# Performance work log

Measured on AMD Instinct MI355X. Metric: run time of the kernel, lower is better.

Reference implementation:

```python
import jax, jax.numpy as jnp
import numpy as np


def setup_inputs() -> dict:
    key = jax.random.key(0)
    ks = jax.random.split(key, 6)
    B, C, H, W = 8, 512, 64, 64
    s = 1.0 / np.sqrt(C)
    return {
        "x": jax.random.normal(ks[0], (B, C, H, W), dtype=jnp.float32),
        "w_phi": jax.random.normal(ks[1], (C, C), dtype=jnp.float32) * s,
        "w_theta": jax.random.normal(ks[2], (C, C), dtype=jnp.float32) * s,
        "w_g": jax.random.normal(ks[3], (C, C), dtype=jnp.float32) * s,
        "w_mask": jax.random.normal(ks[4], (C, C), dtype=jnp.float32) * s,
        "gamma": jax.random.normal(ks[5], (1,), dtype=jnp.float32) * 0.1,
    }


def reference(x, w_phi, w_theta, w_g, w_mask, gamma):
    b, c, h, w = x.shape
    n = h * w
    xf = x.reshape(b, c, n)  # flatten spatial: [b, c, n]
    # 1x1 convs (bias=False) are channel-mixing GEMMs
    phi = jnp.einsum("oc,bcn->bon", w_phi, xf)    # [b, c, n]
    theta = jnp.einsum("oc,bcn->bon", w_theta, xf)  # [b, c, n]
    g = jnp.einsum("oc,bcn->bon", w_g, xf)        # [b, c, n]
    # channel-channel attention (unscaled), softmax over last dim
    attn = jax.nn.softmax(jnp.einsum("bcn,bdn->bcd", phi, theta), axis=-1)  # [b, c, c]
    y = jnp.einsum("bcd,bdn->bcn", attn, g)  # [b, c, n]
    # faithful to torch: permute(0,2,1).contiguous().view(b, c, h, w)
    y = jnp.transpose(y, (0, 2, 1)).reshape(b, c, h, w)
    mask = jnp.einsum("oc,bchw->bohw", w_mask, y)
    return mask * gamma[0] + x
```

## Files before the change

### kernel.cpp

```cpp
#include <hip/hip_runtime.h>
#include <hip/hip_bf16.h>

constexpr int BATCH = 8;
constexpr int C = 512;
constexpr int HW = 4096;
constexpr long CN = (long)C * HW;
constexpr long CC = (long)C * C;

typedef __attribute__((ext_vector_type(8))) short short8;
typedef __attribute__((ext_vector_type(4))) short bf16x4;
typedef __attribute__((ext_vector_type(4))) float f32x4;

__device__ __forceinline__ void gload16(const void* g, void* l) {
  __builtin_amdgcn_global_load_lds(
      (const __attribute__((address_space(1))) void*)g,
      (__attribute__((address_space(3))) void*)l, 16, 0, 0);
}

__device__ __forceinline__ void hilo(float v, __hip_bfloat16& h, __hip_bfloat16& l) {
  h = __float2bfloat16(v);
  l = __float2bfloat16(v - __bfloat162float(h));
}
__device__ __forceinline__ short bfs(float v) {
  __hip_bfloat16 h = __float2bfloat16(v);
  return *(short*)&h;
}

__global__ __launch_bounds__(256) void convx_k(
    const float* __restrict__ x, __hip_bfloat16* __restrict__ xhi,
    __hip_bfloat16* __restrict__ xt) {
  const int b = blockIdx.z;
  const int n0 = blockIdx.x * 64, c0 = blockIdx.y * 64;
  const float* xb = x + (long)b * CN;
  __shared__ short t[64 * 65];
  const int tid = threadIdx.x;
#pragma unroll
  for (int it = 0; it < 2; ++it) {
    int slot = it * 256 + tid;
    int r = slot >> 3, cc = (slot & 7) * 8;
    const float* src = xb + (long)(c0 + r) * HW + n0 + cc;
    f32x4 v0 = *(const f32x4*)src, v1 = *(const f32x4*)(src + 4);
    short8 hh;
#pragma unroll
    for (int e = 0; e < 4; ++e) {
      hh[e] = bfs(v0[e]);
      hh[4 + e] = bfs(v1[e]);
    }
    long idx = (long)b * CN + (long)(c0 + r) * HW + n0 + cc;
    *(short8*)((short*)xhi + idx) = hh;
#pragma unroll
    for (int e = 0; e < 8; ++e) t[r * 65 + cc + e] = hh[e];
  }
  __syncthreads();
#pragma unroll
  for (int it = 0; it < 2; ++it) {
    int slot = it * 256 + tid;
    int r = slot >> 3, cc = (slot & 7) * 8;
    short8 o;
#pragma unroll
    for (int e = 0; e < 8; ++e) o[e] = t[(cc + e) * 65 + r];
    *(short8*)((short*)xt + (long)b * CN + (long)(n0 + r) * C + c0 + cc) = o;
  }
}

__global__ __launch_bounds__(256) void wprep_k(
    const float* __restrict__ wphi, const float* __restrict__ wtheta,
    const float* __restrict__ wg, const float* __restrict__ wmask,
    __hip_bfloat16* __restrict__ wph, __hip_bfloat16* __restrict__ wpl,
    __hip_bfloat16* __restrict__ wth, __hip_bfloat16* __restrict__ wtl,
    __hip_bfloat16* __restrict__ wgT, __hip_bfloat16* __restrict__ wm16) {
  const int z = blockIdx.z;
  const int r0 = blockIdx.y * 64, c0 = blockIdx.x * 64;
  const int tid = threadIdx.x;
  if (z == 2) {
    __shared__ __hip_bfloat16 t[64][65];
#pragma unroll
    for (int i = 0; i < 16; ++i) {
      int e = i * 256 + tid;
      int r = e >> 6, c = e & 63;
      t[r][c] = __float2bfloat16(wg[(long)(r0 + r) * C + c0 + c]);
    }
    __syncthreads();
#pragma unroll
    for (int i = 0; i < 16; ++i) {
      int e = i * 256 + tid;
      int r = e >> 6, c = e & 63;
      wgT[(long)(c0 + r) * C + r0 + c] = t[c][r];
    }
  } else {
#pragma unroll
    for (int i = 0; i < 16; ++i) {
      int e = i * 256 + tid;
      int r = e >> 6, c = e & 63;
      long idx = (long)(r0 + r) * C + c0 + c;
      if (z == 0) {
        __hip_bfloat16 h, l;
        hilo(wphi[idx], h, l);
        wph[idx] = h; wpl[idx] = l;
      } else if (z == 1) {
        __hip_bfloat16 h, l;
        hilo(wtheta[idx], h, l);
        wth[idx] = h; wtl[idx] = l;
      } else {
        wm16[idx] = __float2bfloat16(wmask[idx]);
      }
    }
  }
}

__global__ __launch_bounds__(256) void gram_k(
    const __hip_bfloat16* __restrict__ xhi, float* __restrict__ gpart) {
  const int b = blockIdx.z;
  const int ks = blockIdx.y;
  int i = 0, rem = blockIdx.x;
  while (rem >= 4 - i) { rem -= 4 - i; ++i; }
  const int j = i + rem;
  const int m0 = i * 128, n0 = j * 128;

  const short* X = (const short*)(xhi + (long)b * CN);
  __shared__ short lds[2 * 2 * 128 * 64];
  const int tid = threadIdx.x, w = tid >> 6, lane = tid & 63;

  f32x4 acc[4][4] = {};
  const int wr = (w >> 1) * 64, wc = (w & 1) * 64;
  const int kbeg = ks * 512;

  auto STAGE = [&](int buf, int k0) {
    short* lb = lds + buf * 16384;
#pragma unroll
    for (int it = 0; it < 8; ++it) {
      int slot = (w & 1) * 512 + it * 64 + lane;
      int r = slot >> 3, p = slot & 7, c = p ^ (r & 7);
      int gr = (w < 2) ? (m0 + r) : (n0 + r);
      gload16(X + (long)gr * HW + k0 + c * 8, lb + ((w >> 1) * 1024 + slot) * 8);
    }
  };

  STAGE(0, kbeg);
  asm volatile("s_waitcnt vmcnt(0)" ::: "memory");
  __builtin_amdgcn_s_barrier();

  for (int t = 0; t < 8; ++t) {
    if (t < 7) STAGE((t + 1) & 1, kbeg + (t + 1) * 64);
    const short* lb = lds + (t & 1) * 16384;
#pragma unroll
    for (int kh = 0; kh < 2; ++kh) {
      short8 af[4], bfr[4];
      const int ch = kh * 4 + (lane >> 4);
#pragma unroll
      for (int mi = 0; mi < 4; ++mi) {
        int r = wr + mi * 16 + (lane & 15);
        af[mi] = *(const short8*)(lb + (r * 8 + (ch ^ (r & 7))) * 8);
      }
#pragma unroll
      for (int ni = 0; ni < 4; ++ni) {
        int r = wc + ni * 16 + (lane & 15);
        bfr[ni] = *(const short8*)(lb + 8192 + (r * 8 + (ch ^ (r & 7))) * 8);
      }
#pragma unroll
      for (int mi = 0; mi < 4; ++mi)
#pragma unroll
        for (int ni = 0; ni < 4; ++ni)
          acc[mi][ni] = __builtin_amdgcn_mfma_f32_16x16x32_bf16(af[mi], bfr[ni], acc[mi][ni], 0, 0, 0);
    }
    asm volatile("s_waitcnt vmcnt(0)" ::: "memory");
    __builtin_amdgcn_s_barrier();
  }

  float* P = gpart + ((((long)b * 10 + blockIdx.x) * 8 + ks) << 14);
#pragma unroll
  for (int mi = 0; mi < 4; ++mi)
#pragma unroll
    for (int ni = 0; ni < 4; ++ni)
#pragma unroll
      for (int rr = 0; rr < 4; ++rr) {
        int row = wr + mi * 16 + (lane >> 4) * 4 + rr;
        int col = wc + ni * 16 + (lane & 15);
        P[row * 128 + col] = acc[mi][ni][rr];
      }
}

__global__ __launch_bounds__(256) void gred_k(
    const float* __restrict__ gpart, __hip_bfloat16* __restrict__ gh,
    __hip_bfloat16* __restrict__ gl) {
  const int b = blockIdx.z;
  const int half = blockIdx.y;
  int i = 0, rem = blockIdx.x;
  while (rem >= 4 - i) { rem -= 4 - i; ++i; }
  const int j = i + rem;
  const int m0 = i * 128, n0 = j * 128;
  const float* P = gpart + (((long)b * 10 + blockIdx.x) << 17) + half * 8192;
  __shared__ float T[128][65];
  const int tid = threadIdx.x;
  const long dbase = (long)b * CC;

#pragma unroll
  for (int q = 0; q < 8; ++q) {
    int e = q * 1024 + tid * 4;
    int r = e >> 7, c = e & 127;
    f32x4 s = {};
#pragma unroll
    for (int ks = 0; ks < 8; ++ks) s += *(const f32x4*)(P + (ks << 14) + e);
    bf16x4 hh, ll;
#pragma unroll
    for (int u = 0; u < 4; ++u) {
      __hip_bfloat16 h, l;
      hilo(s[u], h, l);
      hh[u] = *(short*)&h;
      ll[u] = *(short*)&l;
      T[c + u][r] = s[u];
    }
    long idx = dbase + (long)(m0 + half * 64 + r) * 512 + n0 + c;
    *(bf16x4*)((short*)gh + idx) = hh;
    *(bf16x4*)((short*)gl + idx) = ll;
  }
  if (i != j) {
    __syncthreads();
#pragma unroll
    for (int q = 0; q < 8; ++q) {
      int e = q * 1024 + tid * 4;
      int rp = e >> 6, cp = e & 63;
      bf16x4 hh, ll;
#pragma unroll
      for (int u = 0; u < 4; ++u) {
        __hip_bfloat16 h, l;
        hilo(T[rp][cp + u], h, l);
        hh[u] = *(short*)&h;
        ll[u] = *(short*)&l;
      }
      long idx = dbase + (long)(n0 + rp) * 512 + m0 + half * 64 + cp;
      *(bf16x4*)((short*)gh + idx) = hh;
      *(bf16x4*)((short*)gl + idx) = ll;
    }
  }
}

template <int AH, int BH, int EPI>
__global__ __launch_bounds__(256) void nt_small(
    const __hip_bfloat16* __restrict__ Ah_, const __hip_bfloat16* __restrict__ Al_,
    const __hip_bfloat16* __restrict__ Bh_, const __hip_bfloat16* __restrict__ Bl_,
    long aStr, long bStr, void* __restrict__ out1, void* __restrict__ out2) {
  const int b = blockIdx.z;
  const int m0 = blockIdx.y * 64, n0 = blockIdx.x * 64;
  const short* Ahp = (const short*)(Ah_ + (long)b * aStr);
  const short* Alp = AH ? (const short*)(Al_ + (long)b * aStr) : nullptr;
  const short* Bhp = (const short*)(Bh_ + (long)b * bStr);
  const short* Blp = BH ? (const short*)(Bl_ + (long)b * bStr) : nullptr;
  constexpr int PAN = (AH && BH) ? 4 : 2;
  __shared__ short lds[2 * PAN * 4096];
  const int tid = threadIdx.x, w = tid >> 6, lane = tid & 63;

  f32x4 acc[2][2] = {};
  const int wr = (w >> 1) * 32, wc = (w & 1) * 32;

  auto STAGE = [&](int buf, int k0) {
    short* lb = lds + buf * PAN * 4096;
    if constexpr (AH && BH) {
      const short* src = (w == 0) ? Ahp : (w == 1) ? Alp : (w == 2) ? Bhp : Blp;
      const int rowbase = (w & 2) ? n0 : m0;
      short* lt = lb + w * 4096;
#pragma unroll
      for (int it = 0; it < 8; ++it) {
        int slot = it * 64 + lane;
        int r = slot >> 3, p = slot & 7, c = p ^ (r & 7);
        gload16(src + (long)(rowbase + r) * 512 + k0 + c * 8, lt + slot * 8);
      }
    } else {
      const short* src = (w < 2) ? Ahp : Bhp;
      const int rowbase = (w < 2) ? m0 : n0;
      short* lt = lb + (w >> 1) * 4096;
#pragma unroll
      for (int it = 0; it < 4; ++it) {
        int slot = (w & 1) * 256 + it * 64 + lane;
        int r = slot >> 3, p = slot & 7, c = p ^ (r & 7);
        gload16(src + (long)(rowbase + r) * 512 + k0 + c * 8, lt + slot * 8);
      }
    }
  };

  STAGE(0, 0);
  asm volatile("s_waitcnt vmcnt(0)" ::: "memory");
  __builtin_amdgcn_s_barrier();

  for (int t = 0; t < 8; ++t) {
    if (t < 7) STAGE((t + 1) & 1, (t + 1) * 64);
    const short* lb = lds + (t & 1) * PAN * 4096;
#pragma unroll
    for (int kh = 0; kh < 2; ++kh) {
      short8 ah[2], al[2], bh[2], bl[2];
      const int ch = kh * 4 + (lane >> 4);
#pragma unroll
      for (int mi = 0; mi < 2; ++mi) {
        int r = wr + mi * 16 + (lane & 15);
        int off = (r * 8 + (ch ^ (r & 7))) * 8;
        ah[mi] = *(const short8*)(lb + off);
        if constexpr (AH) al[mi] = *(const short8*)(lb + 4096 + off);
      }
#pragma unroll
      for (int ni = 0; ni < 2; ++ni) {
        int r = wc + ni * 16 + (lane & 15);
        int off = (r * 8 + (ch ^ (r & 7))) * 8;
        bh[ni] = *(const short8*)(lb + ((AH && BH) ? 8192 : 4096) + off);
        if constexpr (BH) bl[ni] = *(const short8*)(lb + 12288 + off);
      }
#pragma unroll
      for (int mi = 0; mi < 2; ++mi)
#pragma unroll
        for (int ni = 0; ni < 2; ++ni) {
          acc[mi][ni] = __builtin_amdgcn_mfma_f32_16x16x32_bf16(ah[mi], bh[ni], acc[mi][ni], 0, 0, 0);
          if constexpr (BH)
            acc[mi][ni] = __builtin_amdgcn_mfma_f32_16x16x32_bf16(ah[mi], bl[ni], acc[mi][ni], 0, 0, 0);
          if constexpr (AH)
            acc[mi][ni] = __builtin_amdgcn_mfma_f32_16x16x32_bf16(al[mi], bh[ni], acc[mi][ni], 0, 0, 0);
        }
    }
    asm volatile("s_waitcnt vmcnt(0)" ::: "memory");
    __builtin_amdgcn_s_barrier();
  }

#pragma unroll
  for (int mi = 0; mi < 2; ++mi)
#pragma unroll
    for (int ni = 0; ni < 2; ++ni)
#pragma unroll
      for (int rr = 0; rr < 4; ++rr) {
        int row = m0 + wr + mi * 16 + (lane >> 4) * 4 + rr;
        int col = n0 + wc + ni * 16 + (lane & 15);
        long idx = (long)b * CC + (long)row * 512 + col;
        float v = acc[mi][ni][rr];
        if constexpr (EPI == 0) {
          __hip_bfloat16 h, l;
          hilo(v, h, l);
          ((__hip_bfloat16*)out1)[idx] = h;
          ((__hip_bfloat16*)out2)[idx] = l;
        } else if constexpr (EPI == 1) {
          ((float*)out1)[idx] = v;
        } else {
          ((__hip_bfloat16*)out1)[idx] = __float2bfloat16(v);
        }
      }
}

__global__ __launch_bounds__(256) void softmax_k(const float* __restrict__ a,
                                                 __hip_bfloat16* __restrict__ o) {
  const float* row = a + (long)blockIdx.x * 512;
  __hip_bfloat16* orow = o + (long)blockIdx.x * 512;
  const int t = threadIdx.x;
  float v0 = row[t], v1 = row[t + 256];
  __shared__ float sm[256];
  sm[t] = fmaxf(v0, v1);
  __syncthreads();
  for (int s = 128; s > 0; s >>= 1) {
    if (t < s) sm[t] = fmaxf(sm[t], sm[t + s]);
    __syncthreads();
  }
  float mx = sm[0];
  __syncthreads();
  float e0 = expf(v0 - mx), e1 = expf(v1 - mx);
  sm[t] = e0 + e1;
  __syncthreads();
  for (int s = 128; s > 0; s >>= 1) {
    if (t < s) sm[t] += sm[t + s];
    __syncthreads();
  }
  float inv = 1.0f / sm[0];
  orow[t] = __float2bfloat16(e0 * inv);
  orow[t + 256] = __float2bfloat16(e1 * inv);
}

template <int MODE>
__global__ __launch_bounds__(256) void big_k(
    const __hip_bfloat16* __restrict__ Aw, const __hip_bfloat16* __restrict__ Bm,
    void* __restrict__ Cout, const float* __restrict__ x,
    const float* __restrict__ gammaPtr, long aStride) {
  const int b = blockIdx.z;
  const int lin = ((blockIdx.x & 7) << 4) | (blockIdx.x >> 3);
  const int m0 = (lin & 3) * 128;
  const int n0 = (lin >> 2) * 128;
  const short* A = (const short*)(Aw + (long)b * aStride);
  const short* B = (const short*)(Bm + (long)b * CN);
  __shared__ short lds[2 * 2 * 128 * 64];
  const int tid = threadIdx.x, w = tid >> 6, lane = tid & 63;

  f32x4 acc[4][4] = {};
  const int wr = (w >> 1) * 64, wc = (w & 1) * 64;

  auto STAGE = [&](int buf, int k0) {
    short* lb = lds + buf * 16384;
#pragma unroll
    for (int it = 0; it < 8; ++it) {
      int slot = (w & 1) * 512 + it * 64 + lane;
      int r = slot >> 3, p = slot & 7, c = p ^ (r & 7);
      const short* src;
      long goff;
      if (w < 2) {
        src = A;
        goff = (long)(m0 + r) * 512 + k0 + c * 8;
      } else {
        int gr = (MODE == 0) ? (n0 + (r & 15) * 8 + (r >> 4)) : (n0 + r);
        src = B;
        goff = (long)gr * 512 + k0 + c * 8;
      }
      gload16(src + goff, lb + ((w >> 1) * 1024 + slot) * 8);
    }
  };

  STAGE(0, 0);
  asm volatile("s_waitcnt vmcnt(0)" ::: "memory");
  __builtin_amdgcn_s_barrier();

  for (int t = 0; t < 8; ++t) {
    if (t < 7) STAGE((t + 1) & 1, (t + 1) * 64);
    const short* lb = lds + (t & 1) * 16384;
#pragma unroll
    for (int kh = 0; kh < 2; ++kh) {
      short8 af[4], bfr[4];
      const int ch = kh * 4 + (lane >> 4);
#pragma unroll
      for (int mi = 0; mi < 4; ++mi) {
        int r = wr + mi * 16 + (lane & 15);
        af[mi] = *(const short8*)(lb + (r * 8 + (ch ^ (r & 7))) * 8);
      }
#pragma unroll
      for (int ni = 0; ni < 4; ++ni) {
        int r = wc + ni * 16 + (lane & 15);
        bfr[ni] = *(const short8*)(lb + 8192 + (r * 8 + (ch ^ (r & 7))) * 8);
      }
#pragma unroll
      for (int mi = 0; mi < 4; ++mi)
#pragma unroll
        for (int ni = 0; ni < 4; ++ni)
          acc[mi][ni] = __builtin_amdgcn_mfma_f32_16x16x32_bf16(af[mi], bfr[ni], acc[mi][ni], 0, 0, 0);
    }
    asm volatile("s_waitcnt vmcnt(0)" ::: "memory");
    __builtin_amdgcn_s_barrier();
  }

  if (MODE == 0) {
    __hip_bfloat16* yv = (__hip_bfloat16*)Cout + (long)b * CN;
    const int u = lane & 15;
#pragma unroll
    for (int mi = 0; mi < 4; ++mi)
#pragma unroll
      for (int ni = 0; ni < 4; ++ni) {
        int t = (wc >> 4) + ni;
        long base = ((long)(t * 512 + m0 + wr + mi * 16 + (lane >> 4) * 4)) * 512 +
                    (n0 >> 3) + u;
#pragma unroll
        for (int r = 0; r < 4; ++r)
          yv[base + (long)r * 512] = __float2bfloat16(acc[mi][ni][r]);
      }
  } else {
    float* outp = (float*)Cout + (long)b * CN;
    const float* xb = x + (long)b * CN;
    const float g0 = gammaPtr[0];
#pragma unroll
    for (int mi = 0; mi < 4; ++mi)
#pragma unroll
      for (int ni = 0; ni < 4; ++ni)
#pragma unroll
        for (int r = 0; r < 4; ++r) {
          long idx = (long)(m0 + wr + mi * 16 + (lane >> 4) * 4 + r) * HW +
                     n0 + wc + ni * 16 + (lane & 15);
          outp[idx] = g0 * acc[mi][ni][r] + xb[idx];
        }
  }
}

extern "C" void kernel_launch(void* const* d_in, const int* in_sizes, int n_in,
                              void* d_out, int out_size, void* d_ws, size_t ws_size,
                              hipStream_t stream) {
  const float* x       = (const float*)d_in[0];
  const float* w_phi   = (const float*)d_in[1];
  const float* w_theta = (const float*)d_in[2];
  const float* w_g     = (const float*)d_in[3];
  const float* w_mask  = (const float*)d_in[4];
  const float* gamma   = (const float*)d_in[5];
  float* out = (float*)d_out;

  __hip_bfloat16* xhi = (__hip_bfloat16*)d_ws;
  __hip_bfloat16* xt  = xhi + BATCH * CN;
  __hip_bfloat16* gh  = xt + BATCH * CN;
  __hip_bfloat16* gl  = gh + BATCH * CC;
  __hip_bfloat16* t1h = gl + BATCH * CC;
  __hip_bfloat16* t1l = t1h + BATCH * CC;
  __hip_bfloat16* wph = t1l + BATCH * CC;
  __hip_bfloat16* wpl = wph + CC;
  __hip_bfloat16* wth = wpl + CC;
  __hip_bfloat16* wtl = wth + CC;
  __hip_bfloat16* wgT = wtl + CC;
  __hip_bfloat16* wm16 = wgT + CC;
  float* gpart = (float*)(wm16 + CC);
  float* logits           = (float*)gh;
  __hip_bfloat16* attn16  = t1h;
  __hip_bfloat16* mb16    = t1l;
  __hip_bfloat16* yvT     = xhi;

  convx_k<<<dim3(64, 8, BATCH), 256, 0, stream>>>(x, xhi, xt);
  wprep_k<<<dim3(8, 8, 4), 256, 0, stream>>>(w_phi, w_theta, w_g, w_mask,
                                             wph, wpl, wth, wtl, wgT, wm16);
  gram_k<<<dim3(10, 8, BATCH), 256, 0, stream>>>(xhi, gpart);
  gred_k<<<dim3(10, 2, BATCH), 256, 0, stream>>>(gpart, gh, gl);
  nt_small<1, 1, 0><<<dim3(8, 8, BATCH), 256, 0, stream>>>(
      wph, wpl, gh, gl, 0, CC, t1h, t1l);
  nt_small<1, 1, 1><<<dim3(8, 8, BATCH), 256, 0, stream>>>(
      t1h, t1l, wth, wtl, CC, 0, logits, nullptr);
  softmax_k<<<dim3(BATCH * C), dim3(256), 0, stream>>>(logits, attn16);
  nt_small<0, 0, 2><<<dim3(8, 8, BATCH), 256, 0, stream>>>(
      attn16, nullptr, wgT, nullptr, CC, 0, mb16, nullptr);
  big_k<0><<<dim3(128, 1, BATCH), 256, 0, stream>>>(mb16, xt, yvT, nullptr, nullptr, CC);
  big_k<1><<<dim3(128, 1, BATCH), 256, 0, stream>>>(wm16, yvT, out, x, gamma, 0);
}
```

Baseline: 275.0 us.

## Use four-stage K=32 async LDS pipeline in gram and big GEMMs

Replaces the double-buffered K=64 staging in gram_k and big_k with a four-buffer ring of K=32 stages, prefetching three stages ahead and waiting with partial vmcnt counts instead of draining all loads each iteration. LDS offsets use a new swizzle for 32-wide rows, and per-lane fragment offsets are precomputed once. The gram split-K factor is halved (4 slices of 1024), so gram_k launches fewer blocks and gred_k reduces fewer partials. The goal is more overlap of global-to-LDS loads with MFMA and less partial-sum traffic, at the cost of more barriers per K and lower parallelism in gram_k.

```diff
diff --git a/kernel.cpp b/kernel.cpp
--- a/kernel.cpp
+++ b/kernel.cpp
@@ -25,6 +25,17 @@
   __hip_bfloat16 h = __float2bfloat16(v);
   return *(short*)&h;
 }
+
+__device__ __forceinline__ int cidx32(int r, int ch) {
+  return ((r >> 1) * 8 + ((((r & 1) << 2) | ch) ^ ((r >> 1) & 7))) * 8;
+}
+__device__ __forceinline__ void sdec32(int s, int& r, int& ch) {
+  int R = s >> 3, q = s & 7, v = q ^ (R & 7);
+  r = (R << 1) | (v >> 2);
+  ch = v & 3;
+}
+
+#define WAIT_VM(n) asm volatile("s_waitcnt vmcnt(" #n ")" ::: "memory")
 
 __global__ __launch_bounds__(256) void convx_k(
     const float* __restrict__ x, __hip_bfloat16* __restrict__ xhi,
@@ -112,62 +123,67 @@
     const __hip_bfloat16* __restrict__ xhi, float* __restrict__ gpart) {
   const int b = blockIdx.z;
   const int ks = blockIdx.y;
-  int i = 0, rem = blockIdx.x;
-  while (rem >= 4 - i) { rem -= 4 - i; ++i; }
-  const int j = i + rem;
+  int i = 0, rem0 = blockIdx.x;
+  while (rem0 >= 4 - i) { rem0 -= 4 - i; ++i; }
+  const int j = i + rem0;
   const int m0 = i * 128, n0 = j * 128;
 
   const short* X = (const short*)(xhi + (long)b * CN);
-  __shared__ short lds[2 * 2 * 128 * 64];
+  __shared__ short lds[4 * 8192];
   const int tid = threadIdx.x, w = tid >> 6, lane = tid & 63;
 
   f32x4 acc[4][4] = {};
   const int wr = (w >> 1) * 64, wc = (w & 1) * 64;
-  const int kbeg = ks * 512;
+  const int kbeg = ks * 1024;
+  constexpr int NST = 32;
 
   auto STAGE = [&](int buf, int k0) {
-    short* lb = lds + buf * 16384;
-#pragma unroll
-    for (int it = 0; it < 8; ++it) {
-      int slot = (w & 1) * 512 + it * 64 + lane;
-      int r = slot >> 3, p = slot & 7, c = p ^ (r & 7);
+    short* lb = lds + buf * 8192;
+#pragma unroll
+    for (int it = 0; it < 4; ++it) {
+      int s = (w & 1) * 256 + it * 64 + lane;
+      int r, ch;
+      sdec32(s, r, ch);
       int gr = (w < 2) ? (m0 + r) : (n0 + r);
-      gload16(X + (long)gr * HW + k0 + c * 8, lb + ((w >> 1) * 1024 + slot) * 8);
+      gload16(X + (long)gr * HW + k0 + ch * 8, lb + (w >> 1) * 4096 + s * 8);
     }
   };
 
+  const int chf = lane >> 4, rl = lane & 15;
+  int aoff[4], boff[4];
+#pragma unroll
+  for (int mi = 0; mi < 4; ++mi) aoff[mi] = cidx32(wr + mi * 16 + rl, chf);
+#pragma unroll
+  for (int ni = 0; ni < 4; ++ni) boff[ni] = 4096 + cidx32(wc + ni * 16 + rl, chf);
+
   STAGE(0, kbeg);
-  asm volatile("s_waitcnt vmcnt(0)" ::: "memory");
-  __builtin_amdgcn_s_barrier();
-
-  for (int t = 0; t < 8; ++t) {
-    if (t < 7) STAGE((t + 1) & 1, kbeg + (t + 1) * 64);
-    const short* lb = lds + (t & 1) * 16384;
-#pragma unroll
-    for (int kh = 0; kh < 2; ++kh) {
-      short8 af[4], bfr[4];
-      const int ch = kh * 4 + (lane >> 4);
-#pragma unroll
-      for (int mi = 0; mi < 4; ++mi) {
-        int r = wr + mi * 16 + (lane & 15);
-        af[mi] = *(const short8*)(lb + (r * 8 + (ch ^ (r & 7))) * 8);
-      }
-#pragma unroll
-      for (int ni = 0; ni < 4; ++ni) {
-        int r = wc + ni * 16 + (lane & 15);
-        bfr[ni] = *(const short8*)(lb + 8192 + (r * 8 + (ch ^ (r & 7))) * 8);
-      }
-#pragma unroll
-      for (int mi = 0; mi < 4; ++mi)
-#pragma unroll
-        for (int ni = 0; ni < 4; ++ni)
-          acc[mi][ni] = __builtin_amdgcn_mfma_f32_16x16x32_bf16(af[mi], bfr[ni], acc[mi][ni], 0, 0, 0);
-    }
-    asm volatile("s_waitcnt vmcnt(0)" ::: "memory");
+  STAGE(1, kbeg + 32);
+  STAGE(2, kbeg + 64);
+
+#pragma unroll
+  for (int t = 0; t < NST; ++t) {
+    if (t + 3 < NST) STAGE((t + 3) & 3, kbeg + (t + 3) * 32);
+    const int rm = NST - 1 - t;
+    if (rm >= 3) WAIT_VM(12);
+    else if (rm == 2) WAIT_VM(8);
+    else if (rm == 1) WAIT_VM(4);
+    else WAIT_VM(0);
     __builtin_amdgcn_s_barrier();
-  }
-
-  float* P = gpart + ((((long)b * 10 + blockIdx.x) * 8 + ks) << 14);
+    const short* lb = lds + (t & 3) * 8192;
+    short8 af[4], bfr[4];
+#pragma unroll
+    for (int mi = 0; mi < 4; ++mi) af[mi] = *(const short8*)(lb + aoff[mi]);
+#pragma unroll
+    for (int ni = 0; ni < 4; ++ni) bfr[ni] = *(const short8*)(lb + boff[ni]);
+#pragma unroll
+    for (int mi = 0; mi < 4; ++mi)
+#pragma unroll
+      for (int ni = 0; ni < 4; ++ni)
+        acc[mi][ni] = __builtin_amdgcn_mfma_f32_16x16x32_bf16(af[mi], bfr[ni], acc[mi][ni], 0, 0, 0);
+    __builtin_amdgcn_s_barrier();
+  }
+
+  float* P = gpart + ((((long)b * 10 + blockIdx.x) * 4 + ks) << 14);
 #pragma unroll
   for (int mi = 0; mi < 4; ++mi)
 #pragma unroll
@@ -189,7 +205,7 @@
   while (rem >= 4 - i) { rem -= 4 - i; ++i; }
   const int j = i + rem;
   const int m0 = i * 128, n0 = j * 128;
-  const float* P = gpart + (((long)b * 10 + blockIdx.x) << 17) + half * 8192;
+  const float* P = gpart + (((long)b * 10 + blockIdx.x) << 16) + half * 8192;
   __shared__ float T[128][65];
   const int tid = threadIdx.x;
   const long dbase = (long)b * CC;
@@ -200,7 +216,7 @@
     int r = e >> 7, c = e & 127;
     f32x4 s = {};
 #pragma unroll
-    for (int ks = 0; ks < 8; ++ks) s += *(const f32x4*)(P + (ks << 14) + e);
+    for (int ks = 0; ks < 4; ++ks) s += *(const f32x4*)(P + (ks << 14) + e);
     bf16x4 hh, ll;
 #pragma unroll
     for (int u = 0; u < 4; ++u) {
@@ -379,60 +395,60 @@
   const int n0 = (lin >> 2) * 128;
   const short* A = (const short*)(Aw + (long)b * aStride);
   const short* B = (const short*)(Bm + (long)b * CN);
-  __shared__ short lds[2 * 2 * 128 * 64];
+  __shared__ short lds[4 * 8192];
   const int tid = threadIdx.x, w = tid >> 6, lane = tid & 63;
 
   f32x4 acc[4][4] = {};
   const int wr = (w >> 1) * 64, wc = (w & 1) * 64;
+  constexpr int NST = 16;
 
   auto STAGE = [&](int buf, int k0) {
-    short* lb = lds + buf * 16384;
-#pragma unroll
-    for (int it = 0; it < 8; ++it) {
-      int slot = (w & 1) * 512 + it * 64 + lane;
-      int r = slot >> 3, p = slot & 7, c = p ^ (r & 7);
-      const short* src;
-      long goff;
+    short* lb = lds + buf * 8192;
+#pragma unroll
+    for (int it = 0; it < 4; ++it) {
+      int s = (w & 1) * 256 + it * 64 + lane;
+      int r, ch;
+      sdec32(s, r, ch);
       if (w < 2) {
-        src = A;
-        goff = (long)(m0 + r) * 512 + k0 + c * 8;
+        gload16(A + (long)(m0 + r) * 512 + k0 + ch * 8, lb + s * 8);
       } else {
         int gr = (MODE == 0) ? (n0 + (r & 15) * 8 + (r >> 4)) : (n0 + r);
-        src = B;
-        goff = (long)gr * 512 + k0 + c * 8;
-      }
-      gload16(src + goff, lb + ((w >> 1) * 1024 + slot) * 8);
+        gload16(B + (long)gr * 512 + k0 + ch * 8, lb + 4096 + s * 8);
+      }
     }
   };
 
+  const int chf = lane >> 4, rl = lane & 15;
+  int aoff[4], boff[4];
+#pragma unroll
+  for (int mi = 0; mi < 4; ++mi) aoff[mi] = cidx32(wr + mi * 16 + rl, chf);
+#pragma unroll
+  for (int ni = 0; ni < 4; ++ni) boff[ni] = 4096 + cidx32(wc + ni * 16 + rl, chf);
+
   STAGE(0, 0);
-  asm volatile("s_waitcnt vmcnt(0)" ::: "memory");
-  __builtin_amdgcn_s_barrier();
-
-  for (int t = 0; t < 8; ++t) {
-    if (t < 7) STAGE((t + 1) & 1, (t + 1) * 64);
-    const short* lb = lds + (t & 1) * 16384;
-#pragma unroll
-    for (int kh = 0; kh < 2; ++kh) {
-      short8 af[4], bfr[4];
-      const int ch = kh * 4 + (lane >> 4);
-#pragma unroll
-      for (int mi = 0; mi < 4; ++mi) {
-        int r = wr + mi * 16 + (lane & 15);
-        af[mi] = *(const short8*)(lb + (r * 8 + (ch ^ (r & 7))) * 8);
-      }
-#pragma unroll
-      for (int ni = 0; ni < 4; ++ni) {
-        int r = wc + ni * 16 + (lane & 15);
-        bfr[ni] = *(const short8*)(lb + 8192 + (r * 8 + (ch ^ (r & 7))) * 8);
-      }
-#pragma unroll
-      for (int mi = 0; mi < 4; ++mi)
-#pragma unroll
-        for (int ni = 0; ni < 4; ++ni)
-          acc[mi][ni] = __builtin_amdgcn_mfma_f32_16x16x32_bf16(af[mi], bfr[ni], acc[mi][ni], 0, 0, 0);
-    }
-    asm volatile("s_waitcnt vmcnt(0)" ::: "memory");
+  STAGE(1, 32);
+  STAGE(2, 64);
+
+#pragma unroll
+  for (int t = 0; t < NST; ++t) {
+    if (t + 3 < NST) STAGE((t + 3) & 3, (t + 3) * 32);
+    const int rm = NST - 1 - t;
+    if (rm >= 3) WAIT_VM(12);
+    else if (rm == 2) WAIT_VM(8);
+    else if (rm == 1) WAIT_VM(4);
+    else WAIT_VM(0);
+    __builtin_amdgcn_s_barrier();
+    const short* lb = lds + (t & 3) * 8192;
+    short8 af[4], bfr[4];
+#pragma unroll
+    for (int mi = 0; mi < 4; ++mi) af[mi] = *(const short8*)(lb + aoff[mi]);
+#pragma unroll
+    for (int ni = 0; ni < 4; ++ni) bfr[ni] = *(const short8*)(lb + boff[ni]);
+#pragma unroll
+    for (int mi = 0; mi < 4; ++mi)
+#pragma unroll
+      for (int ni = 0; ni < 4; ++ni)
+        acc[mi][ni] = __builtin_amdgcn_mfma_f32_16x16x32_bf16(af[mi], bfr[ni], acc[mi][ni], 0, 0, 0);
     __builtin_amdgcn_s_barrier();
   }
 
@@ -499,7 +515,7 @@
   convx_k<<<dim3(64, 8, BATCH), 256, 0, stream>>>(x, xhi, xt);
   wprep_k<<<dim3(8, 8, 4), 256, 0, stream>>>(w_phi, w_theta, w_g, w_mask,
                                              wph, wpl, wth, wtl, wgT, wm16);
-  gram_k<<<dim3(10, 8, BATCH), 256, 0, stream>>>(xhi, gpart);
+  gram_k<<<dim3(10, 4, BATCH), 256, 0, stream>>>(xhi, gpart);
   gred_k<<<dim3(10, 2, BATCH), 256, 0, stream>>>(gpart, gh, gl);
   nt_small<1, 1, 0><<<dim3(8, 8, BATCH), 256, 0, stream>>>(
       wph, wpl, gh, gl, 0, CC, t1h, t1l);
```

Measured after the change: 270.4 us. No clear change (-1.7%).
